# Optimization experiments

Measured on AMD Instinct MI355X. Metric: run time of the kernel, lower is better.

The kernel has to match this reference:

```python
import jax, jax.numpy as jnp
import numpy as np

NUM_FEATURES = 256
GROUP_SIZE = 16
NUM_GROUPS = NUM_FEATURES // GROUP_SIZE
EPS = 1e-06


def setup_inputs() -> dict:
    key = jax.random.key(0)
    x = jax.random.normal(key, (32, NUM_FEATURES, 56, 56), dtype=jnp.float32)
    return {"x": x}


def reference(x):
    # Training-mode group whitening (ZCA-via-Cholesky, lower-triangular inverse).
    m, d, h, w = x.shape
    n = m * h * w
    # (d, m, h, w): channels leading, like torch permute(1,0,2,3)
    xt = jnp.transpose(x, (1, 0, 2, 3))
    mu = jnp.mean(xt, axis=(1, 2, 3))                      # per-channel mean
    xc = (xt - mu[:, None, None, None]).reshape(NUM_GROUPS, GROUP_SIZE, n)
    # Batched covariance over each group: (G, gs, gs)
    sigma_hat = jnp.einsum('gin,gjn->gij', xc, xc) / (n - 1)
    eye = jnp.eye(GROUP_SIZE, dtype=x.dtype)
    sigma = (1.0 - EPS) * sigma_hat + EPS * eye
    T = jnp.linalg.cholesky(sigma)                          # lower triangular
    W_b = jnp.linalg.inv(T)
    x_hat = jnp.einsum('gij,gjn->gin', W_b, xc)             # whiten
    x_hat = x_hat.reshape(d, m, h, w)
    return jnp.transpose(x_hat, (1, 0, 2, 3))
```

## Files before the change

kernel.cpp:

```cpp
#include <hip/hip_runtime.h>

#define M_BATCH 32
#define D_FEAT 256
#define HW 3136
#define HW2 1568
#define NGROUPS 16
#define GS 16
#define NTOT (M_BATCH * HW)
#define TRI 136
#define EPS_W 1e-6f

__device__ __host__ constexpr int tidx(int i, int j) { return i * (i + 1) / 2 + j; }

__global__ __launch_bounds__(256, 2) void whiten_stats(const float2* __restrict__ x2,
                                                       float* __restrict__ sums,
                                                       float* __restrict__ gram) {
    const int b = blockIdx.x, g = blockIdx.y;
    const int tid = threadIdx.x, w = tid >> 6, lane = tid & 63;
    const float2* base = x2 + ((size_t)b * D_FEAT + (size_t)g * GS) * HW2;

    float acc[TRI], sv[GS];
#pragma unroll
    for (int k = 0; k < TRI; ++k) acc[k] = 0.0f;
#pragma unroll
    for (int j = 0; j < GS; ++j) sv[j] = 0.0f;

#pragma unroll 1
    for (int p = tid; p < HW2; p += 256) {
        float2 v[GS];
#pragma unroll
        for (int j = 0; j < GS; ++j) v[j] = base[(size_t)j * HW2 + p];
#pragma unroll
        for (int i = 0; i < GS; ++i) {
            sv[i] += v[i].x + v[i].y;
#pragma unroll
            for (int j = 0; j <= i; ++j) {
                float t = acc[tidx(i, j)];
                t = fmaf(v[i].x, v[j].x, t);
                t = fmaf(v[i].y, v[j].y, t);
                acc[tidx(i, j)] = t;
            }
        }
    }

    __shared__ float red[4][TRI + GS];
#pragma unroll
    for (int k = 0; k < TRI; ++k) {
        float r = acc[k];
#pragma unroll
        for (int off = 32; off > 0; off >>= 1) r += __shfl_down(r, off, 64);
        if (lane == 0) red[w][k] = r;
    }
#pragma unroll
    for (int j = 0; j < GS; ++j) {
        float r = sv[j];
#pragma unroll
        for (int off = 32; off > 0; off >>= 1) r += __shfl_down(r, off, 64);
        if (lane == 0) red[w][TRI + j] = r;
    }
    __syncthreads();
    if (tid < TRI) {
        atomicAdd(&gram[g * TRI + tid],
                  red[0][tid] + red[1][tid] + red[2][tid] + red[3][tid]);
    } else if (tid < TRI + GS) {
        atomicAdd(&sums[g * GS + (tid - TRI)],
                  red[0][tid] + red[1][tid] + red[2][tid] + red[3][tid]);
    }
}

__global__ __launch_bounds__(64, 1) void whiten_solve(const float* __restrict__ sums,
                                                      const float* __restrict__ gram,
                                                      float* __restrict__ wout,
                                                      float* __restrict__ muout) {
    const int g = threadIdx.x;
    if (g >= NGROUPS) return;

    float mu[GS];
#pragma unroll
    for (int j = 0; j < GS; ++j) mu[j] = sums[g * GS + j] * (1.0f / (float)NTOT);

    float S[TRI];
#pragma unroll
    for (int i = 0; i < GS; ++i) {
#pragma unroll
        for (int j = 0; j <= i; ++j) {
            float sg = (gram[g * TRI + tidx(i, j)] - (float)NTOT * mu[i] * mu[j])
                       * (1.0f / (float)(NTOT - 1));
            sg *= (1.0f - EPS_W);
            if (i == j) sg += EPS_W;
            S[tidx(i, j)] = sg;
        }
    }

#pragma unroll
    for (int c = 0; c < GS; ++c) {
        float d = S[tidx(c, c)];
#pragma unroll
        for (int k = 0; k < c; ++k) d -= S[tidx(c, k)] * S[tidx(c, k)];
        d = sqrtf(d);
        S[tidx(c, c)] = d;
        const float inv = 1.0f / d;
#pragma unroll
        for (int i = c + 1; i < GS; ++i) {
            float t = S[tidx(i, c)];
#pragma unroll
            for (int k = 0; k < c; ++k) t -= S[tidx(i, k)] * S[tidx(c, k)];
            S[tidx(i, c)] = t * inv;
        }
    }

#pragma unroll
    for (int c = 0; c < GS; ++c) {
        const float wcc = 1.0f / S[tidx(c, c)];
        S[tidx(c, c)] = wcc;
#pragma unroll
        for (int i = c + 1; i < GS; ++i) {
            float a = 0.0f;
#pragma unroll
            for (int k = c; k < i; ++k) a += S[tidx(i, k)] * S[tidx(k, c)];
            S[tidx(i, c)] = -a / S[tidx(i, i)];
        }
    }

#pragma unroll
    for (int k = 0; k < TRI; ++k) wout[g * TRI + k] = S[k];
#pragma unroll
    for (int j = 0; j < GS; ++j) muout[g * GS + j] = mu[j];
}

__global__ __launch_bounds__(256, 2) void whiten_apply(const float2* __restrict__ x2,
                                                       const float* __restrict__ wmat,
                                                       const float* __restrict__ muv,
                                                       float2* __restrict__ out2) {
    const int b = blockIdx.x, g = blockIdx.y;
    const int tid = threadIdx.x;

    float wv[TRI], cb[GS];
#pragma unroll
    for (int k = 0; k < TRI; ++k) wv[k] = wmat[g * TRI + k];
#pragma unroll
    for (int i = 0; i < GS; ++i) {
        float c = 0.0f;
#pragma unroll
        for (int j = 0; j <= i; ++j) c = fmaf(wv[tidx(i, j)], muv[g * GS + j], c);
        cb[i] = c;
    }

    const size_t off0 = ((size_t)b * D_FEAT + (size_t)g * GS) * HW2;
    const float2* base = x2 + off0;
    float2* obase = out2 + off0;

#pragma unroll 1
    for (int p = tid; p < HW2; p += 256) {
        float2 v[GS];
#pragma unroll
        for (int j = 0; j < GS; ++j) v[j] = base[(size_t)j * HW2 + p];
#pragma unroll
        for (int i = 0; i < GS; ++i) {
            float2 o;
            o.x = -cb[i];
            o.y = -cb[i];
#pragma unroll
            for (int j = 0; j <= i; ++j) {
                const float wc = wv[tidx(i, j)];
                o.x = fmaf(wc, v[j].x, o.x);
                o.y = fmaf(wc, v[j].y, o.y);
            }
            obase[(size_t)i * HW2 + p] = o;
        }
    }
}

extern "C" void kernel_launch(void* const* d_in, const int* in_sizes, int n_in,
                              void* d_out, int out_size, void* d_ws, size_t ws_size,
                              hipStream_t stream) {
    const float* x = (const float*)d_in[0];
    float* out = (float*)d_out;

    float* ws = (float*)d_ws;
    float* sums = ws;
    float* gram = ws + 256;
    float* wmat = ws + 256 + 2176;
    float* muv  = wmat + 2176;

    hipMemsetAsync(ws, 0, (256 + 2176) * sizeof(float), stream);

    dim3 grid(M_BATCH, NGROUPS);
    whiten_stats<<<grid, 256, 0, stream>>>((const float2*)x, sums, gram);
    whiten_solve<<<1, 64, 0, stream>>>(sums, gram, wmat, muv);
    whiten_apply<<<grid, 256, 0, stream>>>((const float2*)x, wmat, muv, (float2*)out);
}
```

Before: 250.7 us.

## Stage group tiles through LDS with float4 global loads and stores

Both the statistics and apply kernels now copy each quarter of a group's 16 channels into shared memory using wide float4 global loads, then compute from LDS. The apply kernel also writes its results back into the LDS tile and streams them out as float4 stores. The aim is wider, better-coalesced global transactions and fewer in-flight strided loads per thread. In exchange it adds about 50KB of LDS per block and several barriers per quarter, and within each block global loads no longer overlap with compute.

```diff
diff --git a/kernel.cpp b/kernel.cpp
--- a/kernel.cpp
+++ b/kernel.cpp
@@ -3,21 +3,35 @@
 #define M_BATCH 32
 #define D_FEAT 256
 #define HW 3136
-#define HW2 1568
+#define HW4 784
 #define NGROUPS 16
 #define GS 16
 #define NTOT (M_BATCH * HW)
 #define TRI 136
 #define EPS_W 1e-6f
 
+#define NQ 4
+#define QPOS4 196
+#define QPOS2 392
+#define TILE4 (GS * QPOS4)
+#define NROUND 13
+
 __device__ __host__ constexpr int tidx(int i, int j) { return i * (i + 1) / 2 + j; }
 
-__global__ __launch_bounds__(256, 2) void whiten_stats(const float2* __restrict__ x2,
+__device__ __forceinline__ void bar_lgkm() {
+    asm volatile("s_waitcnt lgkmcnt(0)" ::: "memory");
+    __builtin_amdgcn_s_barrier();
+    __builtin_amdgcn_sched_barrier(0);
+}
+
+__global__ __launch_bounds__(256, 2) void whiten_stats(const float4* __restrict__ x4,
                                                        float* __restrict__ sums,
                                                        float* __restrict__ gram) {
+    __shared__ float4 tile4[TILE4];
+    __shared__ float red[4][TRI + GS];
+    const int tid = threadIdx.x, w = tid >> 6, lane = tid & 63;
     const int b = blockIdx.x, g = blockIdx.y;
-    const int tid = threadIdx.x, w = tid >> 6, lane = tid & 63;
-    const float2* base = x2 + ((size_t)b * D_FEAT + (size_t)g * GS) * HW2;
+    const float4* rbase4 = x4 + ((size_t)b * D_FEAT + (size_t)g * GS) * HW4;
 
     float acc[TRI], sv[GS];
 #pragma unroll
@@ -26,24 +40,44 @@
     for (int j = 0; j < GS; ++j) sv[j] = 0.0f;
 
 #pragma unroll 1
-    for (int p = tid; p < HW2; p += 256) {
-        float2 v[GS];
-#pragma unroll
-        for (int j = 0; j < GS; ++j) v[j] = base[(size_t)j * HW2 + p];
-#pragma unroll
-        for (int i = 0; i < GS; ++i) {
-            sv[i] += v[i].x + v[i].y;
-#pragma unroll
-            for (int j = 0; j <= i; ++j) {
-                float t = acc[tidx(i, j)];
-                t = fmaf(v[i].x, v[j].x, t);
-                t = fmaf(v[i].y, v[j].y, t);
-                acc[tidx(i, j)] = t;
-            }
-        }
-    }
-
-    __shared__ float red[4][TRI + GS];
+    for (int q = 0; q < NQ; ++q) {
+        float4 st[NROUND];
+#pragma unroll
+        for (int r = 0; r < NROUND; ++r) {
+            const int k = tid + r * 256;
+            if (k < TILE4) {
+                const int ch = k / QPOS4, pos = k - ch * QPOS4;
+                st[r] = rbase4[(size_t)ch * HW4 + q * QPOS4 + pos];
+            }
+        }
+        bar_lgkm();
+#pragma unroll
+        for (int r = 0; r < NROUND; ++r) {
+            const int k = tid + r * 256;
+            if (k < TILE4) tile4[k] = st[r];
+        }
+        bar_lgkm();
+
+        const float2* t2 = (const float2*)tile4;
+#pragma unroll 1
+        for (int p = tid; p < QPOS2; p += 256) {
+            float2 v[GS];
+#pragma unroll
+            for (int j = 0; j < GS; ++j) v[j] = t2[j * QPOS2 + p];
+#pragma unroll
+            for (int i = 0; i < GS; ++i) {
+                sv[i] += v[i].x + v[i].y;
+#pragma unroll
+                for (int j = 0; j <= i; ++j) {
+                    float t = acc[tidx(i, j)];
+                    t = fmaf(v[i].x, v[j].x, t);
+                    t = fmaf(v[i].y, v[j].y, t);
+                    acc[tidx(i, j)] = t;
+                }
+            }
+        }
+    }
+
 #pragma unroll
     for (int k = 0; k < TRI; ++k) {
         float r = acc[k];
@@ -128,12 +162,16 @@
     for (int j = 0; j < GS; ++j) muout[g * GS + j] = mu[j];
 }
 
-__global__ __launch_bounds__(256, 2) void whiten_apply(const float2* __restrict__ x2,
+__global__ __launch_bounds__(256, 2) void whiten_apply(const float4* __restrict__ x4,
                                                        const float* __restrict__ wmat,
                                                        const float* __restrict__ muv,
-                                                       float2* __restrict__ out2) {
+                                                       float4* __restrict__ out4) {
+    __shared__ float4 tile4[TILE4];
+    const int tid = threadIdx.x;
     const int b = blockIdx.x, g = blockIdx.y;
-    const int tid = threadIdx.x;
+    const size_t roff = ((size_t)b * D_FEAT + (size_t)g * GS) * HW4;
+    const float4* rbase4 = x4 + roff;
+    float4* obase4 = out4 + roff;
 
     float wv[TRI], cb[GS];
 #pragma unroll
@@ -146,27 +184,57 @@
         cb[i] = c;
     }
 
-    const size_t off0 = ((size_t)b * D_FEAT + (size_t)g * GS) * HW2;
-    const float2* base = x2 + off0;
-    float2* obase = out2 + off0;
-
-#pragma unroll 1
-    for (int p = tid; p < HW2; p += 256) {
-        float2 v[GS];
-#pragma unroll
-        for (int j = 0; j < GS; ++j) v[j] = base[(size_t)j * HW2 + p];
-#pragma unroll
-        for (int i = 0; i < GS; ++i) {
-            float2 o;
-            o.x = -cb[i];
-            o.y = -cb[i];
-#pragma unroll
-            for (int j = 0; j <= i; ++j) {
-                const float wc = wv[tidx(i, j)];
-                o.x = fmaf(wc, v[j].x, o.x);
-                o.y = fmaf(wc, v[j].y, o.y);
-            }
-            obase[(size_t)i * HW2 + p] = o;
+#pragma unroll 1
+    for (int q = 0; q < NQ; ++q) {
+        float4 st[NROUND];
+#pragma unroll
+        for (int r = 0; r < NROUND; ++r) {
+            const int k = tid + r * 256;
+            if (k < TILE4) {
+                const int ch = k / QPOS4, pos = k - ch * QPOS4;
+                st[r] = rbase4[(size_t)ch * HW4 + q * QPOS4 + pos];
+            }
+        }
+        bar_lgkm();
+#pragma unroll
+        for (int r = 0; r < NROUND; ++r) {
+            const int k = tid + r * 256;
+            if (k < TILE4) tile4[k] = st[r];
+        }
+        bar_lgkm();
+
+        {
+            const float2* t2 = (const float2*)tile4;
+            float2* t2w = (float2*)tile4;
+#pragma unroll 1
+            for (int p = tid; p < QPOS2; p += 256) {
+                float2 v[GS];
+#pragma unroll
+                for (int j = 0; j < GS; ++j) v[j] = t2[j * QPOS2 + p];
+#pragma unroll
+                for (int i = 0; i < GS; ++i) {
+                    float2 o;
+                    o.x = -cb[i];
+                    o.y = -cb[i];
+#pragma unroll
+                    for (int j = 0; j <= i; ++j) {
+                        const float wc = wv[tidx(i, j)];
+                        o.x = fmaf(wc, v[j].x, o.x);
+                        o.y = fmaf(wc, v[j].y, o.y);
+                    }
+                    t2w[i * QPOS2 + p] = o;
+                }
+            }
+        }
+        bar_lgkm();
+
+#pragma unroll
+        for (int r = 0; r < NROUND; ++r) {
+            const int k = tid + r * 256;
+            if (k < TILE4) {
+                const int ch = k / QPOS4, pos = k - ch * QPOS4;
+                obase4[(size_t)ch * HW4 + q * QPOS4 + pos] = tile4[k];
+            }
         }
     }
 }
@@ -186,7 +254,7 @@
     hipMemsetAsync(ws, 0, (256 + 2176) * sizeof(float), stream);
 
     dim3 grid(M_BATCH, NGROUPS);
-    whiten_stats<<<grid, 256, 0, stream>>>((const float2*)x, sums, gram);
+    whiten_stats<<<grid, 256, 0, stream>>>((const float4*)x, sums, gram);
     whiten_solve<<<1, 64, 0, stream>>>(sums, gram, wmat, muv);
-    whiten_apply<<<grid, 256, 0, stream>>>((const float2*)x, wmat, muv, (float2*)out);
-}
+    whiten_apply<<<grid, 256, 0, stream>>>((const float4*)x, wmat, muv, (float4*)out);
+}
```

New measurement: 302.4 us. 20.6% more time.
